# Kernel optimization log

Hardware: AMD Instinct MI355X
Metric: run time of the kernel (lower is better)

The kernel has to match this reference:

```python
import math
import jax, jax.numpy as jnp
import numpy as np

HIDDEN_DIM = 256
NEG_INF = -1e30


def setup_inputs() -> dict:
    key = jax.random.key(0)
    k1, k2, k3, k4 = jax.random.split(key, 4)
    B, L_IN, L_MEM, D_IN, D_MEM = 16, 2048, 2048, 512, 512
    inputs = jax.random.normal(k1, (B, L_IN, D_IN), dtype=jnp.float32)
    memory = jax.random.normal(k2, (B, L_MEM, D_MEM), dtype=jnp.float32)
    memory_mask = jnp.ones((B, L_MEM), dtype=jnp.int32)
    W_in = jax.random.normal(k3, (D_IN, HIDDEN_DIM), dtype=jnp.float32) * (1.0 / math.sqrt(D_IN))
    W_mem = jax.random.normal(k4, (D_MEM, HIDDEN_DIM), dtype=jnp.float32) * (1.0 / math.sqrt(D_MEM))
    return {"inputs": inputs, "memory": memory, "memory_mask": memory_mask,
            "W_in": W_in, "W_mem": W_mem}


def reference(inputs, memory, memory_mask, W_in, W_mem):
    # Projections: Linear(bias=False) + ReLU (dropout is identity at drop_prob=0)
    inp_h = jax.nn.relu(jnp.einsum('bld,dh->blh', inputs, W_in))    # [B, L_in, H]
    mem_h = jax.nn.relu(jnp.einsum('bmd,dh->bmh', memory, W_mem))   # [B, L_mem, H]
    # Scaled dot-product scores
    scale = 1.0 / math.sqrt(HIDDEN_DIM)
    logits = jnp.einsum('blh,bmh->blm', inp_h, mem_h) * scale        # [B, L_in, L_mem]
    # Masked softmax over memory axis (mask broadcast over query axis)
    mask = (memory_mask > 0)[:, None, :]                             # [B, 1, L_mem]
    logits = jnp.where(mask, logits, NEG_INF)
    score = jax.nn.softmax(logits, axis=-1)                          # [B, L_in, L_mem]
    # Context over the ORIGINAL (unprojected) memory, then concat with inputs
    context = jnp.einsum('blm,bmd->bld', score, memory)              # [B, L_in, D_mem]
    return jnp.concatenate([context, inputs], axis=-1)               # [B, L_in, D_mem+D_in]
```

## Files before the change

kernel.cpp:

```cpp
#include <hip/hip_runtime.h>
#include <cstdint>
#include <cstddef>

typedef _Float16 f16;
typedef __attribute__((ext_vector_type(4)))  _Float16 f16x4;
typedef __attribute__((ext_vector_type(8)))  _Float16 f16x8;
typedef __attribute__((ext_vector_type(2)))  __fp16   fp16v2;
typedef __attribute__((ext_vector_type(4)))  float    f32x4;
typedef __attribute__((ext_vector_type(16))) float    f32x16;

static constexpr int BB = 16, LL = 2048, DIN = 512, HH = 256, DOUT = 1024;
static constexpr float SCALE = 0.0625f;
#define NEG_BIG (-1e30f)

__device__ __forceinline__ void gload16(const void* g, void* l) {
  __builtin_amdgcn_global_load_lds(
      (const __attribute__((address_space(1))) unsigned int*)g,
      (__attribute__((address_space(3))) unsigned int*)l, 16, 0, 0);
}

__device__ __forceinline__ unsigned pk2(float a, float b) {
  union { fp16v2 v; unsigned u; } c;
  c.v = __builtin_amdgcn_cvt_pkrtz(a, b);
  return c.u;
}

__device__ __forceinline__ float xchg32(float x, int hi) {
  union { float f; unsigned u; } a, b;
  a.f = x; b.f = x;
  asm volatile("v_permlane32_swap_b32 %0, %1" : "+v"(a.u), "+v"(b.u));
  return hi ? a.f : b.f;
}

__global__ void wt_kernel(const float* __restrict__ W, f16* __restrict__ WT) {
  int g = blockIdx.x * 256 + threadIdx.x;
  int d = g >> 8, h = g & 255;
  WT[h * 512 + d] = (f16)W[g];
}

__global__ void vt_kernel(const float* __restrict__ mem, f16* __restrict__ VT) {
  int m0 = blockIdx.x * 32, d0 = blockIdx.y * 32, b = blockIdx.z;
  __shared__ f16 t[32][36];
  int tid = threadIdx.x;
  {
    int r = tid >> 3, c4 = (tid & 7) * 4;
    float4 v = *(const float4*)(mem + (size_t)(b * LL + m0 + r) * DIN + d0 + c4);
    t[c4 + 0][r] = (f16)v.x; t[c4 + 1][r] = (f16)v.y;
    t[c4 + 2][r] = (f16)v.z; t[c4 + 3][r] = (f16)v.w;
  }
  __syncthreads();
  {
    int d = tid >> 3, seg = tid & 7;
    f16x4 hv = *(const f16x4*)&t[d][seg * 4];
    *(f16x4*)(VT + (size_t)(b * 512 + d0 + d) * 2048 + m0 + seg * 4) = hv;
  }
}

__global__ __launch_bounds__(256, 2) void proj_kernel(const float* __restrict__ X,
                                                      const f16* __restrict__ WT,
                                                      f16* __restrict__ Out) {
  const int Rbase = blockIdx.x * 128, Cbase = blockIdx.y * 128;
  __shared__ f16 a_t[128 * 40];
  __shared__ f16 b_t[128 * 32];
  const int tid = threadIdx.x, lane = tid & 63, wave = tid >> 6;
  const int wr = wave >> 1, wc = wave & 1;
  const int l15 = lane & 15, g4 = lane >> 4;
  f32x4 acc[4][4] = {};
  for (int ks = 0; ks < 16; ++ks) {
    __syncthreads();
#pragma unroll
    for (int k = 0; k < 4; ++k) {
      int idx = k * 256 + tid;
      int row = idx >> 3, c4 = idx & 7;
      float4 v = *(const float4*)(X + (size_t)(Rbase + row) * 512 + ks * 32 + c4 * 4);
      f16x4 hv = { (f16)v.x, (f16)v.y, (f16)v.z, (f16)v.w };
      *(f16x4*)((char*)a_t + row * 80 + c4 * 8) = hv;
    }
#pragma unroll
    for (int i = 0; i < 2; ++i) {
      int o = i * 4096 + wave * 1024 + lane * 16;
      int r = o >> 6, cp = o & 63;
      gload16((const char*)WT + (size_t)(Cbase + r) * 1024 + ks * 64 + (cp ^ ((r & 3) << 4)),
              (char*)b_t + i * 4096 + wave * 1024);
    }
    __syncthreads();
    f16x8 af[4], bf[4];
#pragma unroll
    for (int mi = 0; mi < 4; ++mi) {
      int r = wr * 64 + mi * 16 + l15;
      af[mi] = *(const f16x8*)((const char*)a_t + r * 80 + g4 * 16);
    }
#pragma unroll
    for (int ni = 0; ni < 4; ++ni) {
      int r = wc * 64 + ni * 16 + l15;
      bf[ni] = *(const f16x8*)((const char*)b_t + r * 64 + ((g4 * 16) ^ ((r & 3) << 4)));
    }
#pragma unroll
    for (int mi = 0; mi < 4; ++mi)
#pragma unroll
      for (int ni = 0; ni < 4; ++ni)
        acc[mi][ni] = __builtin_amdgcn_mfma_f32_16x16x32_f16(af[mi], bf[ni], acc[mi][ni], 0, 0, 0);
  }
#pragma unroll
  for (int mi = 0; mi < 4; ++mi)
#pragma unroll
    for (int ni = 0; ni < 4; ++ni)
#pragma unroll
      for (int di = 0; di < 4; ++di) {
        int row = Rbase + wr * 64 + mi * 16 + g4 * 4 + di;
        int col = Cbase + wc * 64 + ni * 16 + l15;
        float v = acc[mi][ni][di];
        Out[(size_t)row * 256 + col] = (f16)(v > 0.f ? v : 0.f);
      }
}

__global__ __launch_bounds__(512, 2) void attn_kernel(
    const float* __restrict__ X, const int* __restrict__ mask,
    const f16* __restrict__ Qh, const f16* __restrict__ Kh,
    const f16* __restrict__ VT, float* __restrict__ out) {
  const int blk = blockIdx.x, b = blk >> 4, qbase = (blk & 15) * 128;
  const int tid = threadIdx.x, lane = tid & 63, wave = tid >> 6;
  const int hi = lane >> 5, l31 = lane & 31;
  const int qsub = wave & 3, dvh = wave >> 2;
  __shared__ f16 KtBuf[2][32 * 256];
  __shared__ f16 VtBuf[2][512 * 32];
  __shared__ float Bias[2048];

#pragma unroll
  for (int k = 0; k < 32; ++k) {
    int f4 = k * 512 + tid;
    int row = f4 >> 7, c4 = f4 & 127;
    *(float4*)(out + (size_t)(b * LL + qbase + row) * DOUT + 512 + c4 * 4) =
        *(const float4*)(X + (size_t)(b * LL + qbase + row) * DIN + c4 * 4);
  }
  {
    int4 mv = *(const int4*)(mask + b * LL + tid * 4);
    float4 bv = { mv.x ? 0.f : NEG_BIG, mv.y ? 0.f : NEG_BIG,
                  mv.z ? 0.f : NEG_BIG, mv.w ? 0.f : NEG_BIG };
    *(float4*)&Bias[tid * 4] = bv;
  }

  const int qr = qbase + qsub * 32 + l31;
  f16x8 Qf[16];
  {
    const f16x8* qrow = (const f16x8*)(Qh + (size_t)(b * LL + qr) * HH);
#pragma unroll
    for (int c = 0; c < 16; ++c) Qf[c] = qrow[2 * c + hi];
  }
  f32x16 acc[8] = {};
  float m_run = NEG_BIG, l_run = 0.f;

  auto stage = [&](int bufi, int mbase) {
#pragma unroll
    for (int i = 0; i < 2; ++i) {
      int o = i * 8192 + wave * 1024 + lane * 16;
      int r = o >> 9, cp = o & 511;
      gload16((const char*)Kh + (size_t)(b * LL + mbase + r) * 512 + (cp ^ ((r & 31) << 4)),
              (char*)KtBuf[bufi] + i * 8192 + wave * 1024);
    }
#pragma unroll
    for (int i = 0; i < 4; ++i) {
      int o = i * 8192 + wave * 1024 + lane * 16;
      int dv = o >> 6, cp = o & 63;
      gload16((const char*)VT + (size_t)(b * 512 + dv) * 4096 + mbase * 2 + (cp ^ (((dv >> 1) & 3) << 4)),
              (char*)VtBuf[bufi] + i * 8192 + wave * 1024);
    }
  };

  stage(0, 0);
  __syncthreads();

  for (int mt = 0; mt < 64; ++mt) {
    const int cur = mt & 1;
    const int mbase = mt * 32;
    stage(cur ^ 1, ((mt + 1) & 63) * 32);
    asm volatile("s_waitcnt vmcnt(6)" ::: "memory");
    __builtin_amdgcn_sched_barrier(0);
    __builtin_amdgcn_s_barrier();

    const char* kb = (const char*)KtBuf[cur];
    const char* vb = (const char*)VtBuf[cur];

    f32x16 s0 = {}, s1 = {};
    __builtin_amdgcn_s_setprio(1);
#pragma unroll
    for (int c = 0; c < 8; ++c) {
      f16x8 kf0 = *(const f16x8*)(kb + l31 * 512 + (((2 * c) * 32 + hi * 16) ^ (l31 << 4)));
      f16x8 kf1 = *(const f16x8*)(kb + l31 * 512 + (((2 * c + 1) * 32 + hi * 16) ^ (l31 << 4)));
      s0 = __builtin_amdgcn_mfma_f32_32x32x16_f16(kf0, Qf[2 * c], s0, 0, 0, 0);
      s1 = __builtin_amdgcn_mfma_f32_32x32x16_f16(kf1, Qf[2 * c + 1], s1, 0, 0, 0);
    }
    __builtin_amdgcn_s_setprio(0);
    f32x16 s;
#pragma unroll
    for (int r = 0; r < 16; ++r) s[r] = s0[r] + s1[r];

    float tmax = NEG_BIG;
#pragma unroll
    for (int c2 = 0; c2 < 4; ++c2) {
      f32x4 bv = *(const f32x4*)&Bias[mbase + c2 * 8 + hi * 4];
#pragma unroll
      for (int i = 0; i < 4; ++i) {
        s[4 * c2 + i] = s[4 * c2 + i] * SCALE + bv[i];
      }
      tmax = fmaxf(tmax, fmaxf(fmaxf(s[4*c2+0], s[4*c2+1]), fmaxf(s[4*c2+2], s[4*c2+3])));
    }
    tmax = fmaxf(tmax, xchg32(tmax, hi));
    if (__any(tmax > m_run + 8.f)) {
      float mnew = fmaxf(m_run, tmax);
      float alpha = __expf(m_run - mnew);
      m_run = mnew;
      l_run *= alpha;
#pragma unroll
      for (int r = 0; r < 16; ++r) {
        float ar = __shfl(alpha, (r & 3) + 8 * (r >> 2) + 4 * hi, 32);
#pragma unroll
        for (int t = 0; t < 8; ++t) acc[t][r] *= ar;
      }
    }
    float tsum = 0.f;
#pragma unroll
    for (int r = 0; r < 16; ++r) {
      float e = __expf(s[r] - m_run);
      s[r] = e;
      tsum += e;
    }
    tsum += xchg32(tsum, hi);
    l_run += tsum;

    f16x8 pf[2];
#pragma unroll
    for (int j = 0; j < 2; ++j) {
      unsigned a0 = pk2(s[8*j+0], s[8*j+1]);
      unsigned a1 = pk2(s[8*j+2], s[8*j+3]);
      unsigned b0 = pk2(s[8*j+4], s[8*j+5]);
      unsigned b1 = pk2(s[8*j+6], s[8*j+7]);
      asm volatile("v_permlane32_swap_b32 %0, %1" : "+v"(a0), "+v"(b0));
      asm volatile("v_permlane32_swap_b32 %0, %1" : "+v"(a1), "+v"(b1));
      union { f16x8 v; unsigned u[4]; } un;
      un.u[0] = a0; un.u[1] = a1; un.u[2] = b0; un.u[3] = b1;
      pf[j] = un.v;
    }
    __builtin_amdgcn_s_setprio(1);
#pragma unroll
    for (int j = 0; j < 2; ++j)
#pragma unroll
      for (int t = 0; t < 8; ++t) {
        int dvl = dvh * 256 + t * 32 + l31;
        f16x8 vf = *(const f16x8*)(vb + dvl * 64 + ((j * 32 + hi * 16) ^ (((dvl >> 1) & 3) << 4)));
        acc[t] = __builtin_amdgcn_mfma_f32_32x32x16_f16(pf[j], vf, acc[t], 0, 0, 0);
      }
    __builtin_amdgcn_s_setprio(0);
    __builtin_amdgcn_s_barrier();
  }

  float linv = 1.f / l_run;
  float lr[16];
#pragma unroll
  for (int r = 0; r < 16; ++r) lr[r] = __shfl(linv, (r & 3) + 8 * (r >> 2) + 4 * hi, 32);
#pragma unroll
  for (int t = 0; t < 8; ++t) {
    int dv = dvh * 256 + t * 32 + l31;
#pragma unroll
    for (int r = 0; r < 16; ++r) {
      int q = qbase + qsub * 32 + (r & 3) + 8 * (r >> 2) + 4 * hi;
      out[(size_t)(b * LL + q) * DOUT + dv] = acc[t][r] * lr[r];
    }
  }
}

extern "C" void kernel_launch(void* const* d_in, const int* in_sizes, int n_in,
                              void* d_out, int out_size, void* d_ws, size_t ws_size,
                              hipStream_t stream) {
  const float* inputs = (const float*)d_in[0];
  const float* memory = (const float*)d_in[1];
  const int*   mmask  = (const int*)d_in[2];
  const float* W_in   = (const float*)d_in[3];
  const float* W_mem  = (const float*)d_in[4];
  float* out = (float*)d_out;

  char* ws = (char*)d_ws;
  f16* Qh  = (f16*)ws;
  f16* Kh  = (f16*)(ws + (16u << 20));
  f16* VT  = (f16*)(ws + (32u << 20));
  f16* WTi = (f16*)(ws + (64u << 20));
  f16* WTm = (f16*)(ws + (64u << 20) + (1u << 18));

  wt_kernel<<<512, 256, 0, stream>>>(W_in, WTi);
  wt_kernel<<<512, 256, 0, stream>>>(W_mem, WTm);
  vt_kernel<<<dim3(64, 16, 16), 256, 0, stream>>>(memory, VT);
  proj_kernel<<<dim3(256, 2), 256, 0, stream>>>(inputs, WTi, Qh);
  proj_kernel<<<dim3(256, 2), 256, 0, stream>>>(memory, WTm, Kh);
  attn_kernel<<<256, 512, 0, stream>>>(inputs, mmask, Qh, Kh, VT, out);
}
```

Before: 341.1 us.

## Restructure K/V staging into two-tile unrolled pipeline with quad K buffers

Splits K and V staging into separate routines, gives K four LDS buffers and V two, and unrolls the main loop over pairs of 32-key tiles. Wait counts and barriers are placed so that the next K tiles and V tiles are prefetched while the current pair is computed, with fewer barriers per tile. It uses more LDS for the extra K buffers, which may affect occupancy, and the vmcnt(0) wait inside each pair can expose load latency.

New measurement: 434.5 us. 27.4% more time.

```diff
diff --git a/kernel.cpp b/kernel.cpp
--- a/kernel.cpp
+++ b/kernel.cpp
@@ -12,6 +12,9 @@
 static constexpr int BB = 16, LL = 2048, DIN = 512, HH = 256, DOUT = 1024;
 static constexpr float SCALE = 0.0625f;
 #define NEG_BIG (-1e30f)
+
+#define BAR()    __builtin_amdgcn_s_barrier()
+#define SCHED0() __builtin_amdgcn_sched_barrier(0)
 
 __device__ __forceinline__ void gload16(const void* g, void* l) {
   __builtin_amdgcn_global_load_lds(
@@ -122,9 +125,28 @@
   const int tid = threadIdx.x, lane = tid & 63, wave = tid >> 6;
   const int hi = lane >> 5, l31 = lane & 31;
   const int qsub = wave & 3, dvh = wave >> 2;
-  __shared__ f16 KtBuf[2][32 * 256];
-  __shared__ f16 VtBuf[2][512 * 32];
+  __shared__ f16 Kt[4][32 * 256];
+  __shared__ f16 Vt[2][512 * 32];
   __shared__ float Bias[2048];
+
+  auto stageK = [&](f16* dst, int mbase) {
+#pragma unroll
+    for (int i = 0; i < 2; ++i) {
+      int o = i * 8192 + wave * 1024 + lane * 16;
+      int r = o >> 9, cp = o & 511;
+      gload16((const char*)Kh + (size_t)(b * LL + mbase + r) * 512 + (cp ^ ((r & 31) << 4)),
+              (char*)dst + o);
+    }
+  };
+  auto stageV = [&](f16* dst, int mbase) {
+#pragma unroll
+    for (int i = 0; i < 4; ++i) {
+      int o = i * 8192 + wave * 1024 + lane * 16;
+      int dv = o >> 6, cp = o & 63;
+      gload16((const char*)VT + (size_t)(b * 512 + dv) * 4096 + mbase * 2 + (cp ^ (((dv >> 1) & 3) << 4)),
+              (char*)dst + o);
+    }
+  };
 
 #pragma unroll
   for (int k = 0; k < 32; ++k) {
@@ -139,7 +161,6 @@
                   mv.z ? 0.f : NEG_BIG, mv.w ? 0.f : NEG_BIG };
     *(float4*)&Bias[tid * 4] = bv;
   }
-
   const int qr = qbase + qsub * 32 + l31;
   f16x8 Qf[16];
   {
@@ -150,37 +171,14 @@
   f32x16 acc[8] = {};
   float m_run = NEG_BIG, l_run = 0.f;
 
-  auto stage = [&](int bufi, int mbase) {
-#pragma unroll
-    for (int i = 0; i < 2; ++i) {
-      int o = i * 8192 + wave * 1024 + lane * 16;
-      int r = o >> 9, cp = o & 511;
-      gload16((const char*)Kh + (size_t)(b * LL + mbase + r) * 512 + (cp ^ ((r & 31) << 4)),
-              (char*)KtBuf[bufi] + i * 8192 + wave * 1024);
-    }
-#pragma unroll
-    for (int i = 0; i < 4; ++i) {
-      int o = i * 8192 + wave * 1024 + lane * 16;
-      int dv = o >> 6, cp = o & 63;
-      gload16((const char*)VT + (size_t)(b * 512 + dv) * 4096 + mbase * 2 + (cp ^ (((dv >> 1) & 3) << 4)),
-              (char*)VtBuf[bufi] + i * 8192 + wave * 1024);
-    }
-  };
-
-  stage(0, 0);
   __syncthreads();
 
-  for (int mt = 0; mt < 64; ++mt) {
-    const int cur = mt & 1;
-    const int mbase = mt * 32;
-    stage(cur ^ 1, ((mt + 1) & 63) * 32);
-    asm volatile("s_waitcnt vmcnt(6)" ::: "memory");
-    __builtin_amdgcn_sched_barrier(0);
-    __builtin_amdgcn_s_barrier();
-
-    const char* kb = (const char*)KtBuf[cur];
-    const char* vb = (const char*)VtBuf[cur];
-
+  stageK(&Kt[0][0], 0);
+  stageK(&Kt[1][0], 32);
+  stageV(&Vt[0][0], 0);
+  stageV(&Vt[1][0], 32);
+
+  auto TILE = [&](const char* kb, const char* vb, int mbase) {
     f32x16 s0 = {}, s1 = {};
     __builtin_amdgcn_s_setprio(1);
 #pragma unroll
@@ -200,9 +198,7 @@
     for (int c2 = 0; c2 < 4; ++c2) {
       f32x4 bv = *(const f32x4*)&Bias[mbase + c2 * 8 + hi * 4];
 #pragma unroll
-      for (int i = 0; i < 4; ++i) {
-        s[4 * c2 + i] = s[4 * c2 + i] * SCALE + bv[i];
-      }
+      for (int i = 0; i < 4; ++i) s[4 * c2 + i] = s[4 * c2 + i] * SCALE + bv[i];
       tmax = fmaxf(tmax, fmaxf(fmaxf(s[4*c2+0], s[4*c2+1]), fmaxf(s[4*c2+2], s[4*c2+3])));
     }
     tmax = fmaxf(tmax, xchg32(tmax, hi));
@@ -251,7 +247,22 @@
         acc[t] = __builtin_amdgcn_mfma_f32_32x32x16_f16(pf[j], vf, acc[t], 0, 0, 0);
       }
     __builtin_amdgcn_s_setprio(0);
-    __builtin_amdgcn_s_barrier();
+  };
+
+  for (int p = 0; p < 32; ++p) {
+    const int ma = p * 64, mb = ma + 32;
+    asm volatile("s_waitcnt vmcnt(4) lgkmcnt(0)" ::: "memory");
+    SCHED0(); BAR(); SCHED0();
+    TILE((const char*)&Kt[(2 * p) & 3][0], (const char*)&Vt[0][0], ma);
+    asm volatile("s_waitcnt vmcnt(0) lgkmcnt(0)" ::: "memory");
+    SCHED0(); BAR(); SCHED0();
+    stageV(&Vt[0][0], (ma + 64) & 2047);
+    TILE((const char*)&Kt[(2 * p + 1) & 3][0], (const char*)&Vt[1][0], mb);
+    asm volatile("s_waitcnt lgkmcnt(0)" ::: "memory");
+    SCHED0(); BAR(); SCHED0();
+    stageK(&Kt[(2 * p + 2) & 3][0], (ma + 64) & 2047);
+    stageK(&Kt[(2 * p + 3) & 3][0], (mb + 64) & 2047);
+    stageV(&Vt[1][0], (mb + 64) & 2047);
   }
 
   float linv = 1.f / l_run;
```
